# Performance work log

Hardware: AMD Instinct MI355X
Metric: run time of the kernel (lower is better)

Reference implementation:

```python
import jax, jax.numpy as jnp
import numpy as np

B, N, D, H = 8, 512, 512, 8
DK = D // H
DIM_G = 64
WAVE_LEN = 1000.0


def box_rel_emb(f_g):
    # f_g: (B, N, 4) boxes -> (B, N, N, 64) trigonometric pairwise embedding
    b, n = f_g.shape[0], f_g.shape[1]
    x_min, y_min, x_max, y_max = jnp.split(f_g, 4, axis=-1)  # each (B,N,1)
    cx = (x_min + x_max) * 0.5
    cy = (y_min + y_max) * 0.5
    w = x_max - x_min + 1.0
    h = y_max - y_min + 1.0
    dx = jnp.log(jnp.clip(jnp.abs((cx - cx.reshape(b, 1, n)) / w), 1e-3))
    dy = jnp.log(jnp.clip(jnp.abs((cy - cy.reshape(b, 1, n)) / h), 1e-3))
    dw = jnp.log(w / w.reshape(b, 1, n))
    dh = jnp.log(h / h.reshape(b, 1, n))
    pos = jnp.stack([dx, dy, dw, dh], axis=-1)  # (B,N,N,4)
    nfreq = DIM_G // 8
    feat = jnp.arange(nfreq, dtype=jnp.float32) / nfreq
    dim_mat = 1.0 / (WAVE_LEN ** feat)  # (nfreq,)
    mul = (100.0 * pos)[..., None] * dim_mat  # (B,N,N,4,nfreq)
    mul = mul.reshape(b, n, n, 4 * nfreq)
    return jnp.concatenate([jnp.sin(mul), jnp.cos(mul)], axis=-1)  # (B,N,N,64)


def setup_inputs():
    key = jax.random.key(0)
    ks = jax.random.split(key, 10)
    s = 0.02
    return {
        "input_query": jax.random.normal(ks[0], (B, N, D), jnp.float32),
        "input_key": jax.random.normal(ks[1], (B, N, D), jnp.float32),
        "input_value": jax.random.normal(ks[2], (B, N, D), jnp.float32),
        "input_box": jax.random.uniform(ks[3], (B, N, 4), jnp.float32),
        "Wq": jax.random.normal(ks[4], (D, D), jnp.float32) * s,
        "bq": jnp.zeros((D,), jnp.float32),
        "Wk": jax.random.normal(ks[5], (D, D), jnp.float32) * s,
        "bk": jnp.zeros((D,), jnp.float32),
        "Wv": jax.random.normal(ks[6], (D, D), jnp.float32) * s,
        "bv": jnp.zeros((D,), jnp.float32),
        "Wo": jax.random.normal(ks[7], (D, D), jnp.float32) * s,
        "bo": jnp.zeros((D,), jnp.float32),
        "WGw": jax.random.normal(ks[8], (H, DIM_G), jnp.float32) * s,
        "WGb": jnp.zeros((H,), jnp.float32),
    }


def reference(input_query, input_key, input_value, input_box,
              Wq, bq, Wk, bk, Wv, bv, Wo, bo, WGw, WGb):
    geo = box_rel_emb(input_box)  # (B,N,N,64)
    # 8 per-head (64->1) linears batched into one einsum, then ReLU
    wg = jax.nn.relu(jnp.einsum('bnmg,hg->bhnm', geo, WGw)
                     + WGb[None, :, None, None])  # (B,H,N,N)
    q = (input_query @ Wq.T + bq).reshape(B, N, H, DK).transpose(0, 2, 1, 3)
    k = (input_key @ Wk.T + bk).reshape(B, N, H, DK).transpose(0, 2, 1, 3)
    v = (input_value @ Wv.T + bv).reshape(B, N, H, DK).transpose(0, 2, 1, 3)
    scores = jnp.einsum('bhnd,bhmd->bhnm', q, k) / np.float32(np.sqrt(DK))
    attn = jax.nn.softmax(jnp.log(jnp.clip(wg, 1e-6)) + scores, axis=-1)
    out = jnp.einsum('bhnm,bhmd->bhnd', attn, v)
    out = out.transpose(0, 2, 1, 3).reshape(B, N, D)
    return out @ Wo.T + bo
```

## Files before the change

kernel.cpp:

```cpp
#include <hip/hip_runtime.h>
#include <hip/hip_bf16.h>

#define B_ 8
#define N_ 512
#define D_ 512
#define H_ 8
#define DK_ 64

__device__ constexpr float DMc[8] = {
    1.0f, 0.42169650342905464f, 0.1778279410038923f, 0.07498942093324559f,
    0.03162277660168379f, 0.013335214321633241f, 0.005623413251903491f,
    0.0023713737056616554f};

__device__ inline float bf2f(unsigned short u) {
    unsigned int x = ((unsigned int)u) << 16;
    return __uint_as_float(x);
}

typedef __attribute__((ext_vector_type(8))) short bf8v;
typedef __attribute__((ext_vector_type(4))) float f4v;

union AFrag { bf8v v; unsigned int u[4]; uint2 d[2]; };

__device__ inline unsigned int cvt_pk_bf16(float a, float b) {
    unsigned int r;
    asm("v_cvt_pk_bf16_f32 %0, %1, %2" : "=v"(r) : "v"(a), "v"(b));
    return r;
}

__device__ inline void split_pair(float a, float b, unsigned int& uhi, unsigned int& ulo) {
    const unsigned int uh = cvt_pk_bf16(a, b);
    const float ah = __uint_as_float(uh << 16);
    const float bh = __uint_as_float(uh & 0xFFFF0000u);
    ulo = cvt_pk_bf16(a - ah, b - bh);
    uhi = uh;
}

__global__ __launch_bounds__(256) void k_split_w(
    const float* __restrict__ Wq, const float* __restrict__ Wk,
    const float* __restrict__ Wv, const float* __restrict__ Wo,
    const float* __restrict__ Xq, const float* __restrict__ Xk,
    const float* __restrict__ Xv,
    unsigned short* __restrict__ whl, unsigned short* __restrict__ xb)
{
    const int z = blockIdx.y;
    const int nt = blockIdx.x;
    if (z < 4 && nt >= 32) return;

    const float* W = (z == 0) ? Wq : (z == 1) ? Wk : (z == 2) ? Wv : (z == 3) ? Wo
                   : (z == 4) ? Xq : (z == 5) ? Xk : Xv;

    const int t = threadIdx.x;
    const int row = t >> 4;
    const int ks = t & 15;

    const float* wsrc = W + (size_t)(nt * 16 + row) * 512 + ks * 32;
    float e[32];
#pragma unroll
    for (int i = 0; i < 8; ++i) {
        const float4 v4 = *(const float4*)(wsrc + 4 * i);
        e[4 * i] = v4.x; e[4 * i + 1] = v4.y; e[4 * i + 2] = v4.z; e[4 * i + 3] = v4.w;
    }

    if (z == 2 || z == 3) {
        unsigned short* out = whl + 524288 + (size_t)(z - 2) * 524288;
#pragma unroll
        for (int g = 0; g < 4; ++g) {
            unsigned int h0, l0, h1, l1, h2, l2, h3, l3;
            split_pair(e[4 * g + 0], e[4 * g + 1], h0, l0);
            split_pair(e[4 * g + 2], e[4 * g + 3], h1, l1);
            split_pair(e[16 + 4 * g + 0], e[16 + 4 * g + 1], h2, l2);
            split_pair(e[16 + 4 * g + 2], e[16 + 4 * g + 3], h3, l3);
            const size_t base = ((size_t)(nt * 16 + ks) * 8 + g * 2) * 128 + row * 8;
            *(uint4*)(out + base) = make_uint4(h0, h1, h2, h3);
            *(uint4*)(out + base + 128) = make_uint4(l0, l1, l2, l3);
        }
    } else {
        unsigned short* out = (z < 2) ? whl + (size_t)z * 262144
                                      : xb + (size_t)(z - 4) * 2097152;
#pragma unroll
        for (int g = 0; g < 4; ++g) {
            const unsigned int u0 = cvt_pk_bf16(e[4 * g + 0], e[4 * g + 1]);
            const unsigned int u1 = cvt_pk_bf16(e[4 * g + 2], e[4 * g + 3]);
            const unsigned int u2 = cvt_pk_bf16(e[16 + 4 * g + 0], e[16 + 4 * g + 1]);
            const unsigned int u3 = cvt_pk_bf16(e[16 + 4 * g + 2], e[16 + 4 * g + 3]);
            const size_t base = ((size_t)((nt * 16 + ks) * 4 + g)) * 128 + row * 8;
            *(uint4*)(out + base) = make_uint4(u0, u1, u2, u3);
        }
    }
}

__global__ __launch_bounds__(256, 4) void k_mix(
    const unsigned short* __restrict__ xb, const unsigned short* __restrict__ whl,
    const float* __restrict__ bq, const float* __restrict__ bk, const float* __restrict__ bv,
    unsigned short* __restrict__ oq, unsigned short* __restrict__ ok,
    unsigned short* __restrict__ ov,
    const float* __restrict__ box, const float* __restrict__ WGw,
    const float* __restrict__ WGb, unsigned short* __restrict__ wgc)
{
    __shared__ float S[4][520];

    const int bid = blockIdx.x;
    const int grp = bid / 19;
    const int r19 = bid - grp * 19;
    const int t = threadIdx.x;

    if (r19 < 3) {
        const int zz = r19;
        const int mn = grp;
        const int m0 = (mn & 63) * 64;
        const int n0 = (mn >> 6) * 128;

        const float* bias = (zz == 0) ? bq : (zz == 1) ? bk : bv;
        const unsigned short* xp = xb + (size_t)zz * 2097152;
        const unsigned short* wp = whl + ((zz == 2) ? 524288 : (size_t)zz * 262144);
        const bool vsplit = (zz == 2);

        const int lane = t & 63;
        const int wv = t >> 6;
        const int cl = lane & 15, g = lane >> 4;
        const int wr = wv >> 1, wc = wv & 1;

        f4v acc[2][4];
#pragma unroll
        for (int i = 0; i < 2; ++i)
#pragma unroll
            for (int j = 0; j < 4; ++j) acc[i][j] = (f4v){0.f, 0.f, 0.f, 0.f};

        const int ntb = (n0 >> 4) + wc * 4;
        const int mt0 = (m0 >> 4) + wr * 2;

        for (int k0 = 0; k0 < 512; k0 += 64) {
#pragma unroll
            for (int ks = 0; ks < 2; ++ks) {
                const int kidx = (k0 >> 5) + ks;
                AFrag ah[2];
#pragma unroll
                for (int mt = 0; mt < 2; ++mt)
                    ah[mt].v = *(const bf8v*)(xp +
                        ((size_t)((mt0 + mt) * 16 + kidx) * 4 + g) * 128 + cl * 8);
#pragma unroll
                for (int nt = 0; nt < 4; ++nt) {
                    AFrag bh, bl;
                    if (vsplit) {
                        const size_t be = ((size_t)((ntb + nt) * 16 + kidx) * 8 + g * 2) * 128 +
                                          cl * 8;
                        bh.v = *(const bf8v*)(wp + be);
                        bl.v = *(const bf8v*)(wp + be + 128);
                    } else {
                        const size_t be = ((size_t)((ntb + nt) * 16 + kidx) * 4 + g) * 128 +
                                          cl * 8;
                        bh.v = *(const bf8v*)(wp + be);
                    }
#pragma unroll
                    for (int mt = 0; mt < 2; ++mt) {
                        acc[mt][nt] = __builtin_amdgcn_mfma_f32_16x16x32_bf16(
                            ah[mt].v, bh.v, acc[mt][nt], 0, 0, 0);
                        if (vsplit)
                            acc[mt][nt] = __builtin_amdgcn_mfma_f32_16x16x32_bf16(
                                ah[mt].v, bl.v, acc[mt][nt], 0, 0, 0);
                    }
                }
            }
        }

        const int mbase = m0 + wr * 32;
        const int nb = n0 + wc * 64;

        if (zz == 2) {
#pragma unroll
            for (int mt = 0; mt < 2; ++mt) {
#pragma unroll
                for (int nt = 0; nt < 4; ++nt) {
                    const int m = mbase + mt * 16 + 4 * g;
                    const int n = nb + nt * 16 + cl;
                    const float bb = bias[n];
                    uint2 pk;
                    pk.x = cvt_pk_bf16(acc[mt][nt][0] + bb, acc[mt][nt][1] + bb);
                    pk.y = cvt_pk_bf16(acc[mt][nt][2] + bb, acc[mt][nt][3] + bb);
                    *(uint2*)&ov[(((size_t)(m >> 9) * 8 + (n >> 6)) * 64 + (n & 63)) * 512 +
                                 (m & 511)] = pk;
                }
            }
        } else {
            unsigned short* outp = (zz == 0) ? oq : ok;
            const float sc = (zz == 0) ? 0.125f : 1.0f;
#pragma unroll
            for (int mt = 0; mt < 2; ++mt) {
#pragma unroll
                for (int nt = 0; nt < 4; ++nt) {
                    const int n = nb + nt * 16 + cl;
                    const float bb = bias[n];
#pragma unroll
                    for (int r = 0; r < 4; ++r) {
                        const int m = mbase + mt * 16 + 4 * g + r;
                        outp[(((size_t)(m >> 9) * 8 + (n >> 6)) * 512 + (m & 511)) * 64 +
                             (n & 63)] =
                            (unsigned short)cvt_pk_bf16((acc[mt][nt][r] + bb) * sc, 0.f);
                    }
                }
            }
        }
    } else {
        const int wb = grp * 16 + (r19 - 3);
        const int n = wb & 511;
        const int b = wb >> 9;

        for (int mi = t; mi < 512; mi += 256) {
            const float4 bx = *(const float4*)&box[(size_t)(b * N_ + mi) * 4];
            S[0][mi] = (bx.x + bx.z) * 0.5f;
            S[1][mi] = (bx.y + bx.w) * 0.5f;
            S[2][mi] = __logf(bx.z - bx.x + 1.0f);
            S[3][mi] = __logf(bx.w - bx.y + 1.0f);
        }

        const float4 bn = *(const float4*)&box[(size_t)(b * N_ + n) * 4];
        const float wn = bn.z - bn.x + 1.0f;
        const float hn = bn.w - bn.y + 1.0f;
        const float rwn = 1.0f / wn;
        const float rhn = 1.0f / hn;
        const float cxn = (bn.x + bn.z) * 0.5f;
        const float cyn = (bn.y + bn.w) * 0.5f;
        const float lwn = __logf(wn);
        const float lhn = __logf(hn);

        const int lane = t & 63;
        const int col = lane & 15;
        const int grp2 = lane >> 4;
        const int w = t >> 6;

        AFrag bs, bc;
        if (col < 8) {
            const float* wr2 = WGw + col * 64 + grp2 * 8;
#pragma unroll
            for (int j = 0; j < 4; ++j) {
                bs.u[j] = cvt_pk_bf16(wr2[2 * j], wr2[2 * j + 1]);
                bc.u[j] = cvt_pk_bf16(wr2[32 + 2 * j], wr2[32 + 2 * j + 1]);
            }
        } else {
#pragma unroll
            for (int j = 0; j < 4; ++j) { bs.u[j] = 0u; bc.u[j] = 0u; }
        }
        const float bias = (col < 8) ? WGb[col] : 0.0f;

        const float dn = (grp2 == 0) ? cxn : (grp2 == 1) ? cyn : (grp2 == 2) ? lwn : lhn;
        const float rA = (grp2 == 0) ? rwn : rhn;

        unsigned short* outb = (col < 8)
            ? wgc + ((size_t)(b * H_ + col) * N_ + n) * N_ : wgc;

        __syncthreads();

        float svr[8];
#pragma unroll
        for (int mt = 0; mt < 8; ++mt) svr[mt] = S[grp2][mt * 64 + w * 16 + col];

#pragma unroll
        for (int mt = 0; mt < 8; ++mt) {
            const int m0 = mt * 64 + w * 16;

            const float diff = dn - svr[mt];
            const float posA = __logf(fmaxf(fabsf(diff) * rA, 1e-3f));
            const float pos = (grp2 < 2) ? posA : diff;
            const float p100 = 100.0f * pos;

            float sn[8], cs[8];
#pragma unroll
            for (int j = 0; j < 8; ++j) {
                const float ang = p100 * DMc[j];
                sn[j] = __sinf(ang);
                cs[j] = __cosf(ang);
            }
            AFrag as_, ac_;
#pragma unroll
            for (int j = 0; j < 4; ++j) {
                as_.u[j] = cvt_pk_bf16(sn[2 * j], sn[2 * j + 1]);
                ac_.u[j] = cvt_pk_bf16(cs[2 * j], cs[2 * j + 1]);
            }

            f4v acc = __builtin_amdgcn_mfma_f32_16x16x32_bf16(
                as_.v, bs.v, (f4v){0.f, 0.f, 0.f, 0.f}, 0, 0, 0);
            acc = __builtin_amdgcn_mfma_f32_16x16x32_bf16(ac_.v, bc.v, acc, 0, 0, 0);

            if (col < 8) {
                const int mrow = m0 + grp2 * 4;
                const float v0 = fmaxf(acc[0] + bias, 1e-6f);
                const float v1 = fmaxf(acc[1] + bias, 1e-6f);
                const float v2 = fmaxf(acc[2] + bias, 1e-6f);
                const float v3 = fmaxf(acc[3] + bias, 1e-6f);
                uint2 pk;
                pk.x = cvt_pk_bf16(v0, v1);
                pk.y = cvt_pk_bf16(v2, v3);
                *(uint2*)&outb[mrow] = pk;
            }
        }
    }
}

__global__ __launch_bounds__(256, 2) void k_gemm_o(
    const float* __restrict__ AO, const unsigned short* __restrict__ whl,
    const float* __restrict__ bias, float* __restrict__ outp)
{
    const unsigned short* wp = whl + 1048576;

    const int m0 = blockIdx.x * 32;
    const int n0 = blockIdx.y * 128;
    __shared__ __align__(16) short Al[4096];
    const int t = threadIdx.x;
    const int lane = t & 63;
    const int wv = t >> 6;
    const int cl = lane & 15, g = lane >> 4;
    const int wr = wv >> 1, wc = wv & 1;

    const int srow = t >> 3;
    const int skq = t & 7;
    const int ksub = skq >> 2;
    const int half = (skq >> 1) & 1;
    const int g2b = (skq & 1) * 2;
    const float* xp = AO + (size_t)(m0 + srow) * 512 + skq * 8;
    short* alw = Al + ksub * 2048 + (srow >> 4) * 1024 + (srow & 15) * 8 + half * 4;

    f4v acc[4];
#pragma unroll
    for (int j = 0; j < 4; ++j) acc[j] = (f4v){0.f, 0.f, 0.f, 0.f};
    const int ntb = (n0 >> 4) + wc * 4;

    for (int k0 = 0; k0 < 512; k0 += 64) {
        float4 xl0 = *(const float4*)(xp + k0);
        float4 xl1 = *(const float4*)(xp + k0 + 4);

        AFrag bh0[4], bl0[4];
#pragma unroll
        for (int nt = 0; nt < 4; ++nt) {
            const size_t be = ((size_t)((ntb + nt) * 16 + (k0 >> 5)) * 8 + g * 2) * 128 + cl * 8;
            bh0[nt].v = *(const bf8v*)(wp + be);
            bl0[nt].v = *(const bf8v*)(wp + be + 128);
        }
        __syncthreads();
        {
            unsigned int h0, l0, h1, l1;
            split_pair(xl0.x, xl0.y, h0, l0);
            split_pair(xl0.z, xl0.w, h1, l1);
            *(uint2*)(alw + g2b * 256) = make_uint2(h0, h1);
            *(uint2*)(alw + g2b * 256 + 128) = make_uint2(l0, l1);
            split_pair(xl1.x, xl1.y, h0, l0);
            split_pair(xl1.z, xl1.w, h1, l1);
            *(uint2*)(alw + (g2b + 1) * 256) = make_uint2(h0, h1);
            *(uint2*)(alw + (g2b + 1) * 256 + 128) = make_uint2(l0, l1);
        }
        __syncthreads();
        AFrag bh1[4], bl1[4];
#pragma unroll
        for (int nt = 0; nt < 4; ++nt) {
            const size_t be = ((size_t)((ntb + nt) * 16 + (k0 >> 5) + 1) * 8 + g * 2) * 128 + cl * 8;
            bh1[nt].v = *(const bf8v*)(wp + be);
            bl1[nt].v = *(const bf8v*)(wp + be + 128);
        }
#pragma unroll
        for (int ks = 0; ks < 2; ++ks) {
            AFrag ah, alo;
            {
                short* ap = Al + ks * 2048 + wr * 1024 + g * 256 + cl * 8;
                ah.v = *(const bf8v*)ap;
                alo.v = *(const bf8v*)(ap + 128);
            }
#pragma unroll
            for (int nt = 0; nt < 4; ++nt) {
                const AFrag& bhf = ks ? bh1[nt] : bh0[nt];
                const AFrag& blf = ks ? bl1[nt] : bl0[nt];
                acc[nt] = __builtin_amdgcn_mfma_f32_16x16x32_bf16(ah.v, bhf.v, acc[nt], 0, 0, 0);
                acc[nt] = __builtin_amdgcn_mfma_f32_16x16x32_bf16(alo.v, bhf.v, acc[nt], 0, 0, 0);
                acc[nt] = __builtin_amdgcn_mfma_f32_16x16x32_bf16(ah.v, blf.v, acc[nt], 0, 0, 0);
            }
        }
    }
    const int mbase = m0 + wr * 16;
    const int nb = n0 + wc * 64;
#pragma unroll
    for (int nt = 0; nt < 4; ++nt) {
        const int n = nb + nt * 16 + cl;
        const float bb = bias[n];
#pragma unroll
        for (int r = 0; r < 4; ++r) {
            const int m = mbase + 4 * g + r;
            outp[(size_t)m * 512 + n] = acc[nt][r] + bb;
        }
    }
}

__global__ __launch_bounds__(256, 2) void k_attn(
    const unsigned short* __restrict__ qb_g, const unsigned short* __restrict__ kb_g,
    const unsigned short* __restrict__ vt_g, const unsigned short* __restrict__ wgc,
    float* __restrict__ ao)
{
    const int bid = blockIdx.x;
    const int lid = ((bid & 7) << 6) | (bid >> 3);
    const int qt = lid & 7;
    const int h = (lid >> 3) & 7;
    const int b = lid >> 6;
    const int bh = b * H_ + h;

    const int t = threadIdx.x;
    const int lane = t & 63;
    const int w = t >> 6;
    const int cl = lane & 15;
    const int g = lane >> 4;

    __shared__ __align__(16) short Kf[4][2][64][8];
    __shared__ __align__(16) short Vf[2][4][64][8];
    __shared__ __align__(16) short Wf[4][4][64][4];

    AFrag qf0, qf1;
    {
        const unsigned short* qrow = qb_g + ((size_t)bh * N_ + qt * 64 + w * 16 + cl) * DK_;
        qf0.d[0] = *(const uint2*)&qrow[4 * g];
        qf0.d[1] = *(const uint2*)&qrow[16 + 4 * g];
        qf1.d[0] = *(const uint2*)&qrow[32 + 4 * g];
        qf1.d[1] = *(const uint2*)&qrow[48 + 4 * g];
    }

    const unsigned short* kb_bh = kb_g + (size_t)bh * N_ * DK_;
    const unsigned short* vt_bh = vt_g + (size_t)bh * DK_ * N_;
    const unsigned short* wg_q  = wgc + ((size_t)bh * N_ + qt * 64) * N_;

    const int sr = t >> 2;
    const int sc = t & 3;

#define LOADC(mc)                                                               \
    pfa = *(const uint4*)(kb_bh + (size_t)((mc) + sr) * 64 + sc * 8);           \
    pfb = *(const uint4*)(kb_bh + (size_t)((mc) + sr) * 64 + sc * 8 + 32);      \
    pfc = *(const uint4*)(vt_bh + (size_t)sr * 512 + (mc) + sc * 8);            \
    pfd = *(const uint4*)(vt_bh + (size_t)sr * 512 + (mc) + sc * 8 + 32);       \
    pfe = *(const uint4*)(wg_q + (size_t)sr * 512 + (mc) + sc * 8);             \
    pff = *(const uint4*)(wg_q + (size_t)sr * 512 + (mc) + sc * 8 + 32);

#define STK(v, ci) {                                                            \
    short* d = &Kf[sr >> 4][(ci) >> 2][(sr & 15) + (((ci) & 1) << 5)]           \
                 [(((ci) >> 1) & 1) * 4];                                       \
    *(uint2*)d = make_uint2((v).x, (v).y);                                      \
    *(uint2*)(d + 128) = make_uint2((v).z, (v).w); }
#define STV(v, ci) {                                                            \
    short* d = &Vf[(ci) >> 2][sr >> 4][(sr & 15) + (((ci) & 1) << 5)]           \
                 [(((ci) >> 1) & 1) * 4];                                       \
    *(uint2*)d = make_uint2((v).x, (v).y);                                      \
    *(uint2*)(d + 128) = make_uint2((v).z, (v).w); }
#define STW(v, ci) {                                                            \
    short* d = &Wf[(ci) >> 1][sr >> 4][(sr & 15) + (((ci) & 1) << 5)][0];       \
    *(uint2*)d = make_uint2((v).x, (v).y);                                      \
    *(uint2*)(d + 64) = make_uint2((v).z, (v).w); }

    uint4 pfa, pfb, pfc, pfd, pfe, pff;
    LOADC(0)

    float rsum = 0.f;
    f4v oacc[4] = {(f4v){0.f, 0.f, 0.f, 0.f}, (f4v){0.f, 0.f, 0.f, 0.f},
                   (f4v){0.f, 0.f, 0.f, 0.f}, (f4v){0.f, 0.f, 0.f, 0.f}};

    for (int c = 0; c < 8; ++c) {
        __syncthreads();
        STK(pfa, sc)  STK(pfb, sc + 4)
        STV(pfc, sc)  STV(pfd, sc + 4)
        STW(pfe, sc)  STW(pff, sc + 4)
        __syncthreads();
        if (c < 7) { LOADC((c + 1) * 64) }

#pragma unroll
        for (int hf = 0; hf < 2; ++hf) {
            const bf8v a00 = *(const bf8v*)&Kf[2 * hf][0][lane][0];
            const bf8v a01 = *(const bf8v*)&Kf[2 * hf][1][lane][0];
            const bf8v a10 = *(const bf8v*)&Kf[2 * hf + 1][0][lane][0];
            const bf8v a11 = *(const bf8v*)&Kf[2 * hf + 1][1][lane][0];
            f4v sv0 = __builtin_amdgcn_mfma_f32_16x16x32_bf16(
                a00, qf0.v, (f4v){0.f, 0.f, 0.f, 0.f}, 0, 0, 0);
            sv0 = __builtin_amdgcn_mfma_f32_16x16x32_bf16(a01, qf1.v, sv0, 0, 0, 0);
            f4v sv1 = __builtin_amdgcn_mfma_f32_16x16x32_bf16(
                a10, qf0.v, (f4v){0.f, 0.f, 0.f, 0.f}, 0, 0, 0);
            sv1 = __builtin_amdgcn_mfma_f32_16x16x32_bf16(a11, qf1.v, sv1, 0, 0, 0);

            const uint2 wg0 = *(const uint2*)&Wf[2 * hf][w][lane][0];
            const uint2 wg1 = *(const uint2*)&Wf[2 * hf + 1][w][lane][0];
            float p[8];
            p[0] = bf2f((unsigned short)wg0.x) * __expf(sv0[0]);
            p[1] = bf2f((unsigned short)(wg0.x >> 16)) * __expf(sv0[1]);
            p[2] = bf2f((unsigned short)wg0.y) * __expf(sv0[2]);
            p[3] = bf2f((unsigned short)(wg0.y >> 16)) * __expf(sv0[3]);
            p[4] = bf2f((unsigned short)wg1.x) * __expf(sv1[0]);
            p[5] = bf2f((unsigned short)(wg1.x >> 16)) * __expf(sv1[1]);
            p[6] = bf2f((unsigned short)wg1.y) * __expf(sv1[2]);
            p[7] = bf2f((unsigned short)(wg1.y >> 16)) * __expf(sv1[3]);
            rsum += p[0] + p[1] + p[2] + p[3] + p[4] + p[5] + p[6] + p[7];

            AFrag pa;
            pa.u[0] = cvt_pk_bf16(p[0], p[1]);
            pa.u[1] = cvt_pk_bf16(p[2], p[3]);
            pa.u[2] = cvt_pk_bf16(p[4], p[5]);
            pa.u[3] = cvt_pk_bf16(p[6], p[7]);

#pragma unroll
            for (int db = 0; db < 4; ++db) {
                const bf8v vb = *(const bf8v*)&Vf[hf][db][lane][0];
                oacc[db] = __builtin_amdgcn_mfma_f32_16x16x32_bf16(
                    pa.v, vb, oacc[db], 0, 0, 0);
            }
        }
    }

    rsum += __shfl_xor(rsum, 16);
    rsum += __shfl_xor(rsum, 32);

    float rinv[4];
#pragma unroll
    for (int r = 0; r < 4; ++r) rinv[r] = 1.0f / __shfl(rsum, 4 * g + r);

    const int q0 = qt * 64 + w * 16;
#pragma unroll
    for (int db = 0; db < 4; ++db) {
#pragma unroll
        for (int r = 0; r < 4; ++r) {
            const int qq = q0 + 4 * g + r;
            ao[((size_t)(b * N_ + qq)) * D_ + h * DK_ + db * 16 + cl] = oacc[db][r] * rinv[r];
        }
    }
#undef LOADC
#undef STK
#undef STV
#undef STW
}

extern "C" void kernel_launch(void* const* d_in, const int* in_sizes, int n_in,
                              void* d_out, int out_size, void* d_ws, size_t ws_size,
                              hipStream_t stream) {
    (void)in_sizes; (void)n_in; (void)out_size; (void)ws_size;

    const float* xq  = (const float*)d_in[0];
    const float* xk  = (const float*)d_in[1];
    const float* xv  = (const float*)d_in[2];
    const float* box = (const float*)d_in[3];
    const float* Wq  = (const float*)d_in[4];
    const float* bq  = (const float*)d_in[5];
    const float* Wk  = (const float*)d_in[6];
    const float* bk  = (const float*)d_in[7];
    const float* Wv  = (const float*)d_in[8];
    const float* bv  = (const float*)d_in[9];
    const float* Wo  = (const float*)d_in[10];
    const float* bo  = (const float*)d_in[11];
    const float* WGw = (const float*)d_in[12];
    const float* WGb = (const float*)d_in[13];

    unsigned short* qb  = (unsigned short*)d_ws;
    unsigned short* kb  = qb + (1u << 21);
    unsigned short* vt  = kb + (1u << 21);
    unsigned short* wgc = vt + (1u << 21);
    unsigned short* xb  = (unsigned short*)((char*)d_ws + (44u << 20));
    float* ao = (float*)((char*)d_ws + (44u << 20));
    unsigned short* whl = (unsigned short*)((char*)d_ws + (56u << 20));

    k_split_w<<<dim3(256, 7), 256, 0, stream>>>(Wq, Wk, Wv, Wo, xq, xk, xv, whl, xb);
    k_mix<<<dim3(4864), 256, 0, stream>>>(xb, whl, bq, bk, bv, qb, kb, vt,
                                          box, WGw, WGb, wgc);
    k_attn<<<dim3(512), 256, 0, stream>>>(qb, kb, vt, wgc, ao);
    k_gemm_o<<<dim3(128, 4), 256, 0, stream>>>(ao, whl, bo, (float*)d_out);
}
```

Measured before the change: 90.45 us.

## Fuse input bf16 conversion into projection GEMM, drop separate X pre-pass

The fp32 query/key/value activations are no longer converted to a bf16 tiled buffer in the split kernel. The projection GEMM now reads fp32 rows directly and packs them to bf16 in registers, which removes one full write-plus-read of the three inputs and shrinks the split kernel to weights only. Occupancy hint for the mix kernel is raised to 6 blocks, and sin/cos are computed with a single sincos call. The trade-off is that GEMM A-fragment loads are now strided fp32 reads of twice the bytes, each re-read by the column tiles of every block, and the workspace offset for weights is moved.

```diff
diff --git a/kernel.cpp b/kernel.cpp
--- a/kernel.cpp
+++ b/kernel.cpp
@@ -39,17 +39,12 @@
 __global__ __launch_bounds__(256) void k_split_w(
     const float* __restrict__ Wq, const float* __restrict__ Wk,
     const float* __restrict__ Wv, const float* __restrict__ Wo,
-    const float* __restrict__ Xq, const float* __restrict__ Xk,
-    const float* __restrict__ Xv,
-    unsigned short* __restrict__ whl, unsigned short* __restrict__ xb)
+    unsigned short* __restrict__ whl)
 {
     const int z = blockIdx.y;
+    const float* W = (z == 0) ? Wq : (z == 1) ? Wk : (z == 2) ? Wv : Wo;
+
     const int nt = blockIdx.x;
-    if (z < 4 && nt >= 32) return;
-
-    const float* W = (z == 0) ? Wq : (z == 1) ? Wk : (z == 2) ? Wv : (z == 3) ? Wo
-                   : (z == 4) ? Xq : (z == 5) ? Xk : Xv;
-
     const int t = threadIdx.x;
     const int row = t >> 4;
     const int ks = t & 15;
@@ -62,7 +57,18 @@
         e[4 * i] = v4.x; e[4 * i + 1] = v4.y; e[4 * i + 2] = v4.z; e[4 * i + 3] = v4.w;
     }
 
-    if (z == 2 || z == 3) {
+    if (z < 2) {
+        unsigned short* out = whl + (size_t)z * 262144;
+#pragma unroll
+        for (int g = 0; g < 4; ++g) {
+            const unsigned int u0 = cvt_pk_bf16(e[4 * g + 0], e[4 * g + 1]);
+            const unsigned int u1 = cvt_pk_bf16(e[4 * g + 2], e[4 * g + 3]);
+            const unsigned int u2 = cvt_pk_bf16(e[16 + 4 * g + 0], e[16 + 4 * g + 1]);
+            const unsigned int u3 = cvt_pk_bf16(e[16 + 4 * g + 2], e[16 + 4 * g + 3]);
+            const size_t base = ((size_t)((nt * 16 + ks) * 4 + g)) * 128 + row * 8;
+            *(uint4*)(out + base) = make_uint4(u0, u1, u2, u3);
+        }
+    } else {
         unsigned short* out = whl + 524288 + (size_t)(z - 2) * 524288;
 #pragma unroll
         for (int g = 0; g < 4; ++g) {
@@ -75,23 +81,12 @@
             *(uint4*)(out + base) = make_uint4(h0, h1, h2, h3);
             *(uint4*)(out + base + 128) = make_uint4(l0, l1, l2, l3);
         }
-    } else {
-        unsigned short* out = (z < 2) ? whl + (size_t)z * 262144
-                                      : xb + (size_t)(z - 4) * 2097152;
-#pragma unroll
-        for (int g = 0; g < 4; ++g) {
-            const unsigned int u0 = cvt_pk_bf16(e[4 * g + 0], e[4 * g + 1]);
-            const unsigned int u1 = cvt_pk_bf16(e[4 * g + 2], e[4 * g + 3]);
-            const unsigned int u2 = cvt_pk_bf16(e[16 + 4 * g + 0], e[16 + 4 * g + 1]);
-            const unsigned int u3 = cvt_pk_bf16(e[16 + 4 * g + 2], e[16 + 4 * g + 3]);
-            const size_t base = ((size_t)((nt * 16 + ks) * 4 + g)) * 128 + row * 8;
-            *(uint4*)(out + base) = make_uint4(u0, u1, u2, u3);
-        }
-    }
-}
-
-__global__ __launch_bounds__(256, 4) void k_mix(
-    const unsigned short* __restrict__ xb, const unsigned short* __restrict__ whl,
+    }
+}
+
+__global__ __launch_bounds__(256, 6) void k_mix(
+    const float* __restrict__ Xq, const float* __restrict__ Xk, const float* __restrict__ Xv,
+    const unsigned short* __restrict__ whl,
     const float* __restrict__ bq, const float* __restrict__ bk, const float* __restrict__ bv,
     unsigned short* __restrict__ oq, unsigned short* __restrict__ ok,
     unsigned short* __restrict__ ov,
@@ -111,8 +106,8 @@
         const int m0 = (mn & 63) * 64;
         const int n0 = (mn >> 6) * 128;
 
+        const float* X = (zz == 0) ? Xq : (zz == 1) ? Xk : Xv;
         const float* bias = (zz == 0) ? bq : (zz == 1) ? bk : bv;
-        const unsigned short* xp = xb + (size_t)zz * 2097152;
         const unsigned short* wp = whl + ((zz == 2) ? 524288 : (size_t)zz * 262144);
         const bool vsplit = (zz == 2);
 
@@ -136,9 +131,16 @@
                 const int kidx = (k0 >> 5) + ks;
                 AFrag ah[2];
 #pragma unroll
-                for (int mt = 0; mt < 2; ++mt)
-                    ah[mt].v = *(const bf8v*)(xp +
-                        ((size_t)((mt0 + mt) * 16 + kidx) * 4 + g) * 128 + cl * 8);
+                for (int mt = 0; mt < 2; ++mt) {
+                    const float* xrow = X + (size_t)((mt0 + mt) * 16 + cl) * 512 +
+                                        kidx * 32 + 4 * g;
+                    const float4 x0 = *(const float4*)xrow;
+                    const float4 x1 = *(const float4*)(xrow + 16);
+                    ah[mt].u[0] = cvt_pk_bf16(x0.x, x0.y);
+                    ah[mt].u[1] = cvt_pk_bf16(x0.z, x0.w);
+                    ah[mt].u[2] = cvt_pk_bf16(x1.x, x1.y);
+                    ah[mt].u[3] = cvt_pk_bf16(x1.z, x1.w);
+                }
 #pragma unroll
                 for (int nt = 0; nt < 4; ++nt) {
                     AFrag bh, bl;
@@ -267,9 +269,7 @@
             float sn[8], cs[8];
 #pragma unroll
             for (int j = 0; j < 8; ++j) {
-                const float ang = p100 * DMc[j];
-                sn[j] = __sinf(ang);
-                cs[j] = __cosf(ang);
+                __sincosf(p100 * DMc[j], &sn[j], &cs[j]);
             }
             AFrag as_, ac_;
 #pragma unroll
@@ -551,12 +551,11 @@
     unsigned short* kb  = qb + (1u << 21);
     unsigned short* vt  = kb + (1u << 21);
     unsigned short* wgc = vt + (1u << 21);
-    unsigned short* xb  = (unsigned short*)((char*)d_ws + (44u << 20));
     float* ao = (float*)((char*)d_ws + (44u << 20));
-    unsigned short* whl = (unsigned short*)((char*)d_ws + (56u << 20));
-
-    k_split_w<<<dim3(256, 7), 256, 0, stream>>>(Wq, Wk, Wv, Wo, xq, xk, xv, whl, xb);
-    k_mix<<<dim3(4864), 256, 0, stream>>>(xb, whl, bq, bk, bv, qb, kb, vt,
+    unsigned short* whl = (unsigned short*)((char*)d_ws + (52u << 20));
+
+    k_split_w<<<dim3(32, 4), 256, 0, stream>>>(Wq, Wk, Wv, Wo, whl);
+    k_mix<<<dim3(4864), 256, 0, stream>>>(xq, xk, xv, whl, bq, bk, bv, qb, kb, vt,
                                           box, WGw, WGb, wgc);
     k_attn<<<dim3(512), 256, 0, stream>>>(qb, kb, vt, wgc, ao);
     k_gemm_o<<<dim3(128, 4), 256, 0, stream>>>(ao, whl, bo, (float*)d_out);
```

Result: slower. 108.2 us (+19.7%).
